# Kernel tuning notes

Measured on AMD Instinct MI355X. Metric: run time of the kernel, lower is better.

Reference implementation:

```python
import jax, jax.numpy as jnp
import numpy as np

# ---- config (matches init_kwargs) ----
L_LEVELS = 10          # int(log(8192/16)/log(2)) + 1
LEVEL_DIM = 4
BASE_RES = 16
LOG2_T = 21
BOUND = 2.0            # contract() output bound
DENSITY_BIAS = -1.0
RGB_PADDING = 0.001
DEG_VIEW = 4
PRIME1 = np.uint32(2654435761)
PRIME2 = np.uint32(805459861)


def _grid_meta():
    # torch-ngp GridEncoder layout: per-level scale = base*2^l - 1 (per_level_scale=2),
    # resolution = base*2^l, params = min(2^21, (res+1)^3) rounded up to multiple of 8.
    offsets, scales, res_list, sizes = [0], [], [], []
    for l in range(L_LEVELS):
        res = BASE_RES * (2 ** l)
        scales.append(float(res - 1))
        n = min(2 ** LOG2_T, (res + 1) ** 3)
        n = int(np.ceil(n / 8) * 8)
        res_list.append(res)
        sizes.append(n)
        offsets.append(offsets[-1] + n)
    return scales, res_list, sizes, offsets

GRID_SCALES, GRID_RES, GRID_SIZES, GRID_OFFSETS = _grid_meta()
TOTAL_PARAMS = GRID_OFFSETS[-1]  # 14995560
CORNERS = np.array([[(c >> d) & 1 for d in range(3)] for c in range(8)], dtype=np.int32)


def contract(x):
    # mipnerf360 contraction, output in [-2, 2]
    eps = jnp.finfo(x.dtype).eps
    x_mag_sq = jnp.maximum(eps, jnp.sum(x * x, axis=-1, keepdims=True))
    return jnp.where(x_mag_sq <= 1.0, x, ((2.0 * jnp.sqrt(x_mag_sq) - 1.0) / x_mag_sq) * x)


def pos_enc(x):
    # coord.pos_enc with identity, min_deg=0, max_deg=DEG_VIEW -> dim 3 + 3*2*4 = 27
    scales = 2.0 ** jnp.arange(DEG_VIEW, dtype=x.dtype)
    xb = (x[..., None, :] * scales[:, None]).reshape(x.shape[:-1] + (3 * DEG_VIEW,))
    four = jnp.sin(jnp.concatenate([xb, xb + 0.5 * jnp.pi], axis=-1))
    return jnp.concatenate([x, four], axis=-1)


def grid_encode(x01, embeddings):
    # x01: [N,3] in [0,1]; embeddings: [TOTAL_PARAMS, LEVEL_DIM]
    feats = []
    for l in range(L_LEVELS):
        pos = x01 * GRID_SCALES[l] + 0.5  # align_corners=False
        pos_floor = jnp.floor(pos)
        frac = pos - pos_floor            # trilinear weights, differentiable in x01
        pg = pos_floor.astype(jnp.int32)  # [N,3]
        res1 = GRID_RES[l] + 1
        size = GRID_SIZES[l]
        use_hash = (res1 ** 3) > size
        lvl_emb = embeddings[GRID_OFFSETS[l]:GRID_OFFSETS[l] + size]
        acc = jnp.zeros(x01.shape[:-1] + (LEVEL_DIM,), x01.dtype)
        for c in range(8):
            off = CORNERS[c]
            corner = pg + off[None, :]
            if use_hash:
                cu = corner.astype(jnp.uint32)
                idx = (cu[:, 0] ^ (cu[:, 1] * PRIME1) ^ (cu[:, 2] * PRIME2)) % jnp.uint32(size)
                idx = idx.astype(jnp.int32)
            else:
                idx = corner[:, 0] + corner[:, 1] * res1 + corner[:, 2] * (res1 * res1)
            w = jnp.prod(jnp.where(off[None, :] == 1, frac, 1.0 - frac), axis=-1)  # [N]
            acc = acc + w[:, None] * lvl_emb[idx]
        feats.append(acc)
    return jnp.concatenate(feats, axis=-1)  # [N, 40]


def setup_inputs() -> dict:
    key = jax.random.key(0)
    ks = jax.random.split(key, 10)
    R, S = 2048, 32
    coords = jax.random.normal(ks[0], (R, S, 3), jnp.float32) * 1.5
    viewdirs = jax.random.normal(ks[1], (R, 3), jnp.float32)
    viewdirs = viewdirs / jnp.linalg.norm(viewdirs, axis=-1, keepdims=True)
    embeddings = (jax.random.uniform(ks[2], (TOTAL_PARAMS, LEVEL_DIM), jnp.float32) * 2.0 - 1.0) * 1e-4

    def lin(k, fan_in, fan_out):
        k1, k2 = jax.random.split(k)
        lim = 1.0 / np.sqrt(fan_in)
        w = jax.random.uniform(k1, (fan_in, fan_out), jnp.float32, -lim, lim)
        b = jax.random.uniform(k2, (fan_out,), jnp.float32, -lim, lim)
        return w, b

    w_d1, b_d1 = lin(ks[3], L_LEVELS * LEVEL_DIM, 64)
    w_d2, b_d2 = lin(ks[4], 64, 256)
    DIR_DIM = 3 + 3 * 2 * DEG_VIEW  # 27
    w_r0, b_r0 = lin(ks[5], 256 + DIR_DIM, 256)          # 283 -> 256
    w_r1, b_r1 = lin(ks[6], 256 + 256 + DIR_DIM, 256)    # skip concat: 539 -> 256
    w_rgb, b_rgb = lin(ks[7], 256, 3)
    return dict(coords=coords, viewdirs=viewdirs, embeddings=embeddings,
                w_d1=w_d1, b_d1=b_d1, w_d2=w_d2, b_d2=b_d2,
                w_r0=w_r0, b_r0=b_r0, w_r1=w_r1, b_r1=b_r1,
                w_rgb=w_rgb, b_rgb=b_rgb)


def reference(coords, viewdirs, embeddings, w_d1, b_d1, w_d2, b_d2,
              w_r0, b_r0, w_r1, b_r1, w_rgb, b_rgb):
    shape = coords.shape[:-1]  # (rays, samples)
    cw = contract(coords) / BOUND          # coords_warped, in [-1, 1]
    x01 = (cw.reshape(-1, 3) + BOUND) / (2.0 * BOUND)  # encoder normalization with bound=2
    feats = grid_encode(x01, embeddings)               # [N, 40]
    h = jax.nn.relu(feats @ w_d1 + b_d1)
    x = h @ w_d2 + b_d2                                # [N, 256]
    raw_density = x[:, 0].reshape(shape)
    density = jax.nn.softplus(raw_density + DENSITY_BIAS)
    bottleneck = x.reshape(shape + (256,))
    dir_enc = pos_enc(viewdirs)                        # [rays, 27]
    dir_enc = jnp.broadcast_to(dir_enc[..., None, :], shape + (dir_enc.shape[-1],))
    inp = jnp.concatenate([bottleneck, dir_enc], axis=-1)  # [rays, S, 283]
    y = jax.nn.relu(inp @ w_r0 + b_r0)
    y = jnp.concatenate([y, inp], axis=-1)             # skip at layer i == skip_layer_dir == 0
    y = jax.nn.relu(y @ w_r1 + b_r1)
    rgb = jax.nn.sigmoid(y @ w_rgb + b_rgb)            # rgb_premultiplier=1, rgb_bias=0
    rgb = rgb * (1.0 + 2.0 * RGB_PADDING) - RGB_PADDING
    return cw, density, rgb
```

## Files before the change

kernel.cpp:

```cpp
#include <hip/hip_runtime.h>
#include <math.h>

#define NS 65536
#define NRAYS 2048

typedef __attribute__((ext_vector_type(8))) short short8;
typedef __attribute__((ext_vector_type(4))) float f32x4;
typedef unsigned short u16;

#define OFF_FEATS 0ull
#define OFF_HBF   10485760ull
#define OFF_XBF   18874368ull
#define OFF_YBF   52428800ull
#define OFF_DW0   85983232ull
#define OFF_DW1   88080384ull
#define OFF_WD2T  90177536ull
#define OFF_WR0T  90210304ull
#define OFF_WR1T  90341376ull

#define OUT_DENS 196608
#define OUT_RGB  262144

__device__ __forceinline__ u16 f2b(float f) {
    unsigned u = __builtin_bit_cast(unsigned, f);
    return (u16)((u + 0x7FFFu + ((u >> 16) & 1u)) >> 16);
}

__global__ __launch_bounds__(256) void cvt_weights(
    const float* __restrict__ w_d2, const float* __restrict__ w_r0,
    const float* __restrict__ w_r1, u16* __restrict__ wd2t,
    u16* __restrict__ wr0t, u16* __restrict__ wr1t)
{
    int idx = blockIdx.x * 256 + threadIdx.x;
    if (idx < 16384)  wd2t[idx] = f2b(w_d2[(idx & 63)  * 256 + (idx >> 6)]);
    if (idx < 65536)  wr0t[idx] = f2b(w_r0[(idx & 255) * 256 + (idx >> 8)]);
    if (idx < 131072) wr1t[idx] = f2b(w_r1[(idx & 511) * 256 + (idx >> 9)]);
}

__global__ __launch_bounds__(256) void dir_kernel(
    const float* __restrict__ viewdirs,
    const float* __restrict__ w_r0, const float* __restrict__ b_r0,
    const float* __restrict__ w_r1, const float* __restrict__ b_r1,
    float* __restrict__ dirW0, float* __restrict__ dirW1)
{
    __shared__ float de[27];
    int ray = blockIdx.x, t = threadIdx.x;
    if (t < 27) {
        float v;
        if (t < 3) v = viewdirs[3*ray + t];
        else {
            int k = (t - 3) % 12;
            float b = viewdirs[3*ray + (k % 3)] * (float)(1 << (k / 3));
            v = (t < 15) ? sinf(b) : sinf(b + 1.5707964f);
        }
        de[t] = v;
    }
    __syncthreads();
    float a0 = b_r0[t], a1 = b_r1[t];
#pragma unroll
    for (int d = 0; d < 27; ++d) {
        a0 = fmaf(de[d], w_r0[(256+d)*256 + t], a0);
        a1 = fmaf(de[d], w_r1[(512+d)*256 + t], a1);
    }
    dirW0[ray*256 + t] = a0;
    dirW1[ray*256 + t] = a1;
}

__global__ __launch_bounds__(256) void encode_kernel(
    const float* __restrict__ coords, const float* __restrict__ emb,
    float* __restrict__ cw_out, float* __restrict__ featsT)
{
    int t = threadIdx.x;
    int l = blockIdx.x >> 8;
    int i = ((blockIdx.x & 255) << 8) + t;
    float x = coords[3*i], y = coords[3*i+1], z = coords[3*i+2];
    float m2 = fmaxf(x*x + y*y + z*z, 1.1920928955078125e-07f);
    float cx = x, cy = y, cz = z;
    if (m2 > 1.0f) { float s = (2.0f*sqrtf(m2) - 1.0f)/m2; cx*=s; cy*=s; cz*=s; }
    cx *= 0.5f; cy *= 0.5f; cz *= 0.5f;
    if (l == 0) { cw_out[3*i]=cx; cw_out[3*i+1]=cy; cw_out[3*i+2]=cz; }
    float u0 = (cx + 2.0f)*0.25f, u1 = (cy + 2.0f)*0.25f, u2 = (cz + 2.0f)*0.25f;

    int res = 16 << l;
    int res1 = res + 1;
    float scale = (float)(res - 1);
    unsigned off = (l >= 3) ? 315496u + (unsigned)(l-3)*2097152u
                            : (l == 0 ? 0u : (l == 1 ? 4920u : 40864u));
    float p0 = u0*scale + 0.5f, p1 = u1*scale + 0.5f, p2 = u2*scale + 0.5f;
    float f0 = floorf(p0), f1 = floorf(p1), f2 = floorf(p2);
    float fr0 = p0-f0, fr1 = p1-f1, fr2 = p2-f2;
    unsigned g0 = (unsigned)(int)f0, g1 = (unsigned)(int)f1, g2 = (unsigned)(int)f2;
    float a0=0.f, a1=0.f, a2=0.f, a3=0.f;
    bool use_hash = (l >= 3);
#pragma unroll
    for (int c = 0; c < 8; ++c) {
        unsigned ox = c & 1u, oy = (c >> 1) & 1u, oz = (c >> 2) & 1u;
        unsigned qx = g0 + ox, qy = g1 + oy, qz = g2 + oz;
        unsigned idx;
        if (use_hash) idx = (qx ^ (qy*2654435761u) ^ (qz*805459861u)) & 2097151u;
        else          idx = qx + qy*(unsigned)res1 + qz*(unsigned)(res1*res1);
        const float4 e = *(const float4*)(emb + 4u*(off + idx));
        float w = (ox ? fr0 : 1.0f-fr0) * (oy ? fr1 : 1.0f-fr1) * (oz ? fr2 : 1.0f-fr2);
        a0 = fmaf(w, e.x, a0); a1 = fmaf(w, e.y, a1);
        a2 = fmaf(w, e.z, a2); a3 = fmaf(w, e.w, a3);
    }
    featsT[(4*l+0)*NS + i] = a0;
    featsT[(4*l+1)*NS + i] = a1;
    featsT[(4*l+2)*NS + i] = a2;
    featsT[(4*l+3)*NS + i] = a3;
}

__global__ __launch_bounds__(256) void gemm_d1_kernel(
    const float* __restrict__ featsT, const float* __restrict__ w_d1,
    const float* __restrict__ b_d1, const float* __restrict__ w_d2,
    const float* __restrict__ b_d2, u16* __restrict__ h_bf,
    float* __restrict__ dens)
{
    __shared__ float As[40][256];
    __shared__ float Ws[40*64];
    __shared__ float wc0[64];
    int t = threadIdx.x;
    int m0 = blockIdx.x * 256;
#pragma unroll
    for (int k = 0; k < 40; ++k) As[k][t] = featsT[k*NS + m0 + t];
#pragma unroll
    for (int i = 0; i < 10; ++i) Ws[i*256 + t] = w_d1[i*256 + t];
    if (t < 64) wc0[t] = w_d2[t*256];
    __syncthreads();
    int tn = t & 3, tm = t >> 2;
    float acc[4][16] = {};
#pragma unroll
    for (int k = 0; k < 40; ++k) {
        float4 a = *(const float4*)&As[k][tm*4];
        float av[4] = {a.x, a.y, a.z, a.w};
        const float4* wp = (const float4*)&Ws[k*64 + tn*16];
#pragma unroll
        for (int r = 0; r < 4; ++r) {
            float4 w = wp[r];
            float wv[4] = {w.x, w.y, w.z, w.w};
#pragma unroll
            for (int ii = 0; ii < 4; ++ii)
#pragma unroll
                for (int cc = 0; cc < 4; ++cc)
                    acc[ii][r*4+cc] = fmaf(av[ii], wv[cc], acc[ii][r*4+cc]);
        }
    }
    float p[4] = {0.f, 0.f, 0.f, 0.f};
#pragma unroll
    for (int jj = 0; jj < 16; ++jj) {
        int j = tn*16 + jj;
        float bj = b_d1[j], w0 = wc0[j];
#pragma unroll
        for (int ii = 0; ii < 4; ++ii) {
            float h = fmaxf(acc[ii][jj] + bj, 0.f);
            acc[ii][jj] = h;
            p[ii] = fmaf(h, w0, p[ii]);
        }
    }
#pragma unroll
    for (int ii = 0; ii < 4; ++ii) {
        int s = m0 + tm*4 + ii;
        unsigned u[8];
#pragma unroll
        for (int q = 0; q < 8; ++q)
            u[q] = (unsigned)f2b(acc[ii][2*q]) | ((unsigned)f2b(acc[ii][2*q+1]) << 16);
        uint4 v0 = {u[0], u[1], u[2], u[3]};
        uint4 v1 = {u[4], u[5], u[6], u[7]};
        *(uint4*)(h_bf + (size_t)s*64 + tn*16)     = v0;
        *(uint4*)(h_bf + (size_t)s*64 + tn*16 + 8) = v1;
    }
#pragma unroll
    for (int ii = 0; ii < 4; ++ii) {
        p[ii] += __shfl_xor(p[ii], 1, 64);
        p[ii] += __shfl_xor(p[ii], 2, 64);
    }
    if (tn == 0) {
        float b0 = b_d2[0];
#pragma unroll
        for (int ii = 0; ii < 4; ++ii) {
            float z = p[ii] + b0 - 1.0f;
            dens[m0 + tm*4 + ii] = fmaxf(z, 0.f) + log1pf(expf(-fabsf(z)));
        }
    }
}

#define MFMA __builtin_amdgcn_mfma_f32_16x16x32_bf16

__global__ __launch_bounds__(256) void mfma_d2(
    const u16* __restrict__ h_bf, const u16* __restrict__ wt,
    const float* __restrict__ b_d2, u16* __restrict__ xbf)
{
    int t = threadIdx.x, lane = t & 63, w = t >> 6;
    int m0 = blockIdx.x*128 + w*32;
    int rl = lane & 15, kg = (lane >> 4) * 8;
    f32x4 zero = {0.f,0.f,0.f,0.f};
    f32x4 acc[2][16];
#pragma unroll
    for (int a = 0; a < 2; ++a)
#pragma unroll
        for (int b = 0; b < 16; ++b) acc[a][b] = zero;
    const u16* pA0 = h_bf + (size_t)(m0 + rl)*64 + kg;
    const u16* pA1 = h_bf + (size_t)(m0 + 16 + rl)*64 + kg;
    const u16* pB  = wt + rl*64 + kg;
#pragma unroll
    for (int ks = 0; ks < 2; ++ks) {
        int kb = ks*32;
        short8 a0 = *(const short8*)(pA0 + kb);
        short8 a1 = *(const short8*)(pA1 + kb);
#pragma unroll
        for (int nt = 0; nt < 16; ++nt) {
            short8 b = *(const short8*)(pB + nt*1024 + kb);
            acc[0][nt] = MFMA(a0, b, acc[0][nt], 0, 0, 0);
            acc[1][nt] = MFMA(a1, b, acc[1][nt], 0, 0, 0);
        }
    }
    int ro = (lane >> 4) * 4;
#pragma unroll
    for (int nt = 0; nt < 16; ++nt) {
        int col = nt*16 + rl;
        float bias = b_d2[col];
#pragma unroll
        for (int mt = 0; mt < 2; ++mt)
#pragma unroll
            for (int r = 0; r < 4; ++r)
                xbf[(size_t)(m0 + mt*16 + ro + r)*256 + col] = f2b(acc[mt][nt][r] + bias);
    }
}

__global__ __launch_bounds__(256) void mfma_r0(
    const u16* __restrict__ xbf, const u16* __restrict__ wt,
    const float* __restrict__ dirW0, u16* __restrict__ ybf)
{
    int t = threadIdx.x, lane = t & 63, w = t >> 6;
    int m0 = blockIdx.x*128 + w*32;
    int rl = lane & 15, kg = (lane >> 4) * 8;
    f32x4 zero = {0.f,0.f,0.f,0.f};
    f32x4 acc[2][16];
#pragma unroll
    for (int a = 0; a < 2; ++a)
#pragma unroll
        for (int b = 0; b < 16; ++b) acc[a][b] = zero;
    const u16* pA0 = xbf + (size_t)(m0 + rl)*256 + kg;
    const u16* pA1 = xbf + (size_t)(m0 + 16 + rl)*256 + kg;
    const u16* pB  = wt + rl*256 + kg;
#pragma unroll
    for (int ks = 0; ks < 8; ++ks) {
        int kb = ks*32;
        short8 a0 = *(const short8*)(pA0 + kb);
        short8 a1 = *(const short8*)(pA1 + kb);
#pragma unroll
        for (int nt = 0; nt < 16; ++nt) {
            short8 b = *(const short8*)(pB + nt*4096 + kb);
            acc[0][nt] = MFMA(a0, b, acc[0][nt], 0, 0, 0);
            acc[1][nt] = MFMA(a1, b, acc[1][nt], 0, 0, 0);
        }
    }
    const float* dir = dirW0 + (m0 >> 5)*256;
    int ro = (lane >> 4) * 4;
#pragma unroll
    for (int nt = 0; nt < 16; ++nt) {
        int col = nt*16 + rl;
        float bias = dir[col];
#pragma unroll
        for (int mt = 0; mt < 2; ++mt)
#pragma unroll
            for (int r = 0; r < 4; ++r)
                ybf[(size_t)(m0 + mt*16 + ro + r)*256 + col] =
                    f2b(fmaxf(acc[mt][nt][r] + bias, 0.f));
    }
}

__global__ __launch_bounds__(256) void mfma_r1(
    const u16* __restrict__ ybf, const u16* __restrict__ xbf,
    const u16* __restrict__ wt, const float* __restrict__ dirW1,
    const float* __restrict__ w_rgb, const float* __restrict__ b_rgb,
    float* __restrict__ rgb)
{
    int t = threadIdx.x, lane = t & 63, w = t >> 6;
    int m0 = blockIdx.x*128 + w*32;
    int rl = lane & 15, kg = (lane >> 4) * 8;
    f32x4 zero = {0.f,0.f,0.f,0.f};
    f32x4 acc[2][16];
#pragma unroll
    for (int a = 0; a < 2; ++a)
#pragma unroll
        for (int b = 0; b < 16; ++b) acc[a][b] = zero;
    const u16* pAy0 = ybf + (size_t)(m0 + rl)*256 + kg;
    const u16* pAy1 = ybf + (size_t)(m0 + 16 + rl)*256 + kg;
    const u16* pAx0 = xbf + (size_t)(m0 + rl)*256 + kg;
    const u16* pAx1 = xbf + (size_t)(m0 + 16 + rl)*256 + kg;
    const u16* pB   = wt + rl*512 + kg;
#pragma unroll
    for (int ks = 0; ks < 16; ++ks) {
        int kb = ks*32;
        int kl = (ks & 7)*32;
        short8 a0 = (ks < 8) ? *(const short8*)(pAy0 + kl) : *(const short8*)(pAx0 + kl);
        short8 a1 = (ks < 8) ? *(const short8*)(pAy1 + kl) : *(const short8*)(pAx1 + kl);
#pragma unroll
        for (int nt = 0; nt < 16; ++nt) {
            short8 b = *(const short8*)(pB + nt*8192 + kb);
            acc[0][nt] = MFMA(a0, b, acc[0][nt], 0, 0, 0);
            acc[1][nt] = MFMA(a1, b, acc[1][nt], 0, 0, 0);
        }
    }
    const float* dir = dirW1 + (m0 >> 5)*256;
    float p[2][4][3];
#pragma unroll
    for (int mt = 0; mt < 2; ++mt)
#pragma unroll
        for (int r = 0; r < 4; ++r)
            p[mt][r][0] = p[mt][r][1] = p[mt][r][2] = 0.f;
#pragma unroll
    for (int nt = 0; nt < 16; ++nt) {
        int col = nt*16 + rl;
        float dv = dir[col];
        float w0 = w_rgb[col*3], w1 = w_rgb[col*3+1], w2 = w_rgb[col*3+2];
#pragma unroll
        for (int mt = 0; mt < 2; ++mt)
#pragma unroll
            for (int r = 0; r < 4; ++r) {
                float y1 = fmaxf(acc[mt][nt][r] + dv, 0.f);
                p[mt][r][0] = fmaf(y1, w0, p[mt][r][0]);
                p[mt][r][1] = fmaf(y1, w1, p[mt][r][1]);
                p[mt][r][2] = fmaf(y1, w2, p[mt][r][2]);
            }
    }
#pragma unroll
    for (int mask = 1; mask < 16; mask <<= 1)
#pragma unroll
        for (int mt = 0; mt < 2; ++mt)
#pragma unroll
            for (int r = 0; r < 4; ++r)
#pragma unroll
                for (int c = 0; c < 3; ++c)
                    p[mt][r][c] += __shfl_xor(p[mt][r][c], mask, 64);
    if (rl == 0) {
        int ro = (lane >> 4) * 4;
#pragma unroll
        for (int mt = 0; mt < 2; ++mt)
#pragma unroll
            for (int r = 0; r < 4; ++r) {
                int row = m0 + mt*16 + ro + r;
#pragma unroll
                for (int c = 0; c < 3; ++c) {
                    float v = p[mt][r][c] + b_rgb[c];
                    float sg = 1.0f / (1.0f + expf(-v));
                    rgb[row*3 + c] = sg * 1.002f - 0.001f;
                }
            }
    }
}

extern "C" void kernel_launch(void* const* d_in, const int* in_sizes, int n_in,
                              void* d_out, int out_size, void* d_ws, size_t ws_size,
                              hipStream_t stream)
{
    const float* coords   = (const float*)d_in[0];
    const float* viewdirs = (const float*)d_in[1];
    const float* emb      = (const float*)d_in[2];
    const float* w_d1     = (const float*)d_in[3];
    const float* b_d1     = (const float*)d_in[4];
    const float* w_d2     = (const float*)d_in[5];
    const float* b_d2     = (const float*)d_in[6];
    const float* w_r0     = (const float*)d_in[7];
    const float* b_r0     = (const float*)d_in[8];
    const float* w_r1     = (const float*)d_in[9];
    const float* b_r1     = (const float*)d_in[10];
    const float* w_rgb    = (const float*)d_in[11];
    const float* b_rgb    = (const float*)d_in[12];

    float* out  = (float*)d_out;
    float* cw   = out;
    float* dens = out + OUT_DENS;
    float* rgb  = out + OUT_RGB;

    char* wsB = (char*)d_ws;
    float* featsT = (float*)(wsB + OFF_FEATS);
    u16*   h_bf   = (u16*)(wsB + OFF_HBF);
    u16*   xbf    = (u16*)(wsB + OFF_XBF);
    u16*   ybf    = (u16*)(wsB + OFF_YBF);
    float* dirW0  = (float*)(wsB + OFF_DW0);
    float* dirW1  = (float*)(wsB + OFF_DW1);
    u16*   wd2t   = (u16*)(wsB + OFF_WD2T);
    u16*   wr0t   = (u16*)(wsB + OFF_WR0T);
    u16*   wr1t   = (u16*)(wsB + OFF_WR1T);

    cvt_weights<<<512, 256, 0, stream>>>(w_d2, w_r0, w_r1, wd2t, wr0t, wr1t);
    dir_kernel<<<NRAYS, 256, 0, stream>>>(viewdirs, w_r0, b_r0, w_r1, b_r1, dirW0, dirW1);
    encode_kernel<<<2560, 256, 0, stream>>>(coords, emb, cw, featsT);
    gemm_d1_kernel<<<NS/256, 256, 0, stream>>>(featsT, w_d1, b_d1, w_d2, b_d2, h_bf, dens);
    mfma_d2<<<NS/128, 256, 0, stream>>>(h_bf, wd2t, b_d2, xbf);
    mfma_r0<<<NS/128, 256, 0, stream>>>(xbf, wr0t, dirW0, ybf);
    mfma_r1<<<NS/128, 256, 0, stream>>>(ybf, xbf, wr1t, dirW1, w_rgb, b_rgb, rgb);
}
```

Baseline: 508.9 us.

## Fuse r0 and r1 MLP layers via LDS-staged activations; coalesce d2 stores

```diff
diff --git a/kernel.cpp b/kernel.cpp
--- a/kernel.cpp
+++ b/kernel.cpp
@@ -11,7 +11,6 @@
 #define OFF_FEATS 0ull
 #define OFF_HBF   10485760ull
 #define OFF_XBF   18874368ull
-#define OFF_YBF   52428800ull
 #define OFF_DW0   85983232ull
 #define OFF_DW1   88080384ull
 #define OFF_WD2T  90177536ull
@@ -190,6 +189,7 @@
     const u16* __restrict__ h_bf, const u16* __restrict__ wt,
     const float* __restrict__ b_d2, u16* __restrict__ xbf)
 {
+    __shared__ u16 xt[4][8192];
     int t = threadIdx.x, lane = t & 63, w = t >> 6;
     int m0 = blockIdx.x*128 + w*32;
     int rl = lane & 15, kg = (lane >> 4) * 8;
@@ -215,6 +215,7 @@
         }
     }
     int ro = (lane >> 4) * 4;
+    u16* xw = xt[w];
 #pragma unroll
     for (int nt = 0; nt < 16; ++nt) {
         int col = nt*16 + rl;
@@ -222,104 +223,127 @@
 #pragma unroll
         for (int mt = 0; mt < 2; ++mt)
 #pragma unroll
-            for (int r = 0; r < 4; ++r)
-                xbf[(size_t)(m0 + mt*16 + ro + r)*256 + col] = f2b(acc[mt][nt][r] + bias);
-    }
-}
-
-__global__ __launch_bounds__(256) void mfma_r0(
-    const u16* __restrict__ xbf, const u16* __restrict__ wt,
-    const float* __restrict__ dirW0, u16* __restrict__ ybf)
-{
+            for (int r = 0; r < 4; ++r) {
+                int row = mt*16 + ro + r;
+                unsigned byte = (unsigned)(row*512 + col*2) ^ ((unsigned)(row & 7) << 4);
+                xw[byte >> 1] = f2b(acc[mt][nt][r] + bias);
+            }
+    }
+#pragma unroll
+    for (int it = 0; it < 16; ++it) {
+        unsigned flat = it*1024u + (unsigned)lane*16u;
+        unsigned row = flat >> 9, off = flat & 511u;
+        unsigned lb = flat ^ ((row & 7u) << 4);
+        short8 v = *(const short8*)((const char*)xw + lb);
+        *(short8*)(xbf + (size_t)(m0 + row)*256 + (off >> 1)) = v;
+    }
+}
+
+__global__ __launch_bounds__(256) void mfma_tail(
+    const u16* __restrict__ xbf, const u16* __restrict__ w0t,
+    const u16* __restrict__ w1t, const float* __restrict__ dirW0,
+    const float* __restrict__ dirW1, const float* __restrict__ w_rgb,
+    const float* __restrict__ b_rgb, float* __restrict__ rgb)
+{
+    __shared__ u16 yt[4][8192];
     int t = threadIdx.x, lane = t & 63, w = t >> 6;
     int m0 = blockIdx.x*128 + w*32;
     int rl = lane & 15, kg = (lane >> 4) * 8;
+    int ro = (lane >> 4) * 4;
     f32x4 zero = {0.f,0.f,0.f,0.f};
-    f32x4 acc[2][16];
-#pragma unroll
-    for (int a = 0; a < 2; ++a)
-#pragma unroll
-        for (int b = 0; b < 16; ++b) acc[a][b] = zero;
     const u16* pA0 = xbf + (size_t)(m0 + rl)*256 + kg;
     const u16* pA1 = xbf + (size_t)(m0 + 16 + rl)*256 + kg;
-    const u16* pB  = wt + rl*256 + kg;
-#pragma unroll
-    for (int ks = 0; ks < 8; ++ks) {
-        int kb = ks*32;
-        short8 a0 = *(const short8*)(pA0 + kb);
-        short8 a1 = *(const short8*)(pA1 + kb);
+
+    f32x4 acc0[2][16];
+#pragma unroll
+    for (int a = 0; a < 2; ++a)
+#pragma unroll
+        for (int b = 0; b < 16; ++b) acc0[a][b] = zero;
+    {
+        const u16* pB = w0t + rl*256 + kg;
+#pragma unroll
+        for (int ks = 0; ks < 8; ++ks) {
+            int kb = ks*32;
+            short8 a0 = *(const short8*)(pA0 + kb);
+            short8 a1 = *(const short8*)(pA1 + kb);
+#pragma unroll
+            for (int nt = 0; nt < 16; ++nt) {
+                short8 b = *(const short8*)(pB + nt*4096 + kb);
+                acc0[0][nt] = MFMA(a0, b, acc0[0][nt], 0, 0, 0);
+                acc0[1][nt] = MFMA(a1, b, acc0[1][nt], 0, 0, 0);
+            }
+        }
+    }
+    {
+        const float* dir0 = dirW0 + (m0 >> 5)*256;
+        u16* yw = yt[w];
 #pragma unroll
         for (int nt = 0; nt < 16; ++nt) {
-            short8 b = *(const short8*)(pB + nt*4096 + kb);
-            acc[0][nt] = MFMA(a0, b, acc[0][nt], 0, 0, 0);
-            acc[1][nt] = MFMA(a1, b, acc[1][nt], 0, 0, 0);
-        }
-    }
-    const float* dir = dirW0 + (m0 >> 5)*256;
-    int ro = (lane >> 4) * 4;
+            int col = nt*16 + rl;
+            float bias = dir0[col];
+#pragma unroll
+            for (int mt = 0; mt < 2; ++mt)
+#pragma unroll
+                for (int r = 0; r < 4; ++r) {
+                    int row = mt*16 + ro + r;
+                    unsigned byte = (unsigned)(row*512 + col*2) ^ ((unsigned)(row & 7) << 4);
+                    yw[byte >> 1] = f2b(fmaxf(acc0[mt][nt][r] + bias, 0.f));
+                }
+        }
+    }
+    f32x4 acc1[2][16];
+#pragma unroll
+    for (int a = 0; a < 2; ++a)
+#pragma unroll
+        for (int b = 0; b < 16; ++b) acc1[a][b] = zero;
+    {
+        const u16* pB = w1t + rl*512;
+        const char* ywc = (const char*)yt[w];
+        unsigned sw = ((unsigned)(rl & 7)) << 4;
+#pragma unroll
+        for (int ks = 0; ks < 8; ++ks) {
+            int kb = ks*32;
+            unsigned base = (unsigned)((kb + kg)*2);
+            short8 a0 = *(const short8*)(ywc + (((unsigned)(rl*512)       + base) ^ sw));
+            short8 a1 = *(const short8*)(ywc + (((unsigned)((16+rl)*512)  + base) ^ sw));
+#pragma unroll
+            for (int nt = 0; nt < 16; ++nt) {
+                short8 b = *(const short8*)(pB + nt*8192 + kg + kb);
+                acc1[0][nt] = MFMA(a0, b, acc1[0][nt], 0, 0, 0);
+                acc1[1][nt] = MFMA(a1, b, acc1[1][nt], 0, 0, 0);
+            }
+        }
+#pragma unroll
+        for (int ks = 8; ks < 16; ++ks) {
+            int kb = ks*32;
+            int kl = kb - 256;
+            short8 a0 = *(const short8*)(pA0 + kl);
+            short8 a1 = *(const short8*)(pA1 + kl);
+#pragma unroll
+            for (int nt = 0; nt < 16; ++nt) {
+                short8 b = *(const short8*)(pB + nt*8192 + kg + kb);
+                acc1[0][nt] = MFMA(a0, b, acc1[0][nt], 0, 0, 0);
+                acc1[1][nt] = MFMA(a1, b, acc1[1][nt], 0, 0, 0);
+            }
+        }
+    }
+    const float* dir1 = dirW1 + (m0 >> 5)*256;
+    float p[2][4][3];
+#pragma unroll
+    for (int mt = 0; mt < 2; ++mt)
+#pragma unroll
+        for (int r = 0; r < 4; ++r)
+            p[mt][r][0] = p[mt][r][1] = p[mt][r][2] = 0.f;
 #pragma unroll
     for (int nt = 0; nt < 16; ++nt) {
         int col = nt*16 + rl;
-        float bias = dir[col];
+        float dv = dir1[col];
+        float w0 = w_rgb[col*3], w1 = w_rgb[col*3+1], w2 = w_rgb[col*3+2];
 #pragma unroll
         for (int mt = 0; mt < 2; ++mt)
 #pragma unroll
-            for (int r = 0; r < 4; ++r)
-                ybf[(size_t)(m0 + mt*16 + ro + r)*256 + col] =
-                    f2b(fmaxf(acc[mt][nt][r] + bias, 0.f));
-    }
-}
-
-__global__ __launch_bounds__(256) void mfma_r1(
-    const u16* __restrict__ ybf, const u16* __restrict__ xbf,
-    const u16* __restrict__ wt, const float* __restrict__ dirW1,
-    const float* __restrict__ w_rgb, const float* __restrict__ b_rgb,
-    float* __restrict__ rgb)
-{
-    int t = threadIdx.x, lane = t & 63, w = t >> 6;
-    int m0 = blockIdx.x*128 + w*32;
-    int rl = lane & 15, kg = (lane >> 4) * 8;
-    f32x4 zero = {0.f,0.f,0.f,0.f};
-    f32x4 acc[2][16];
-#pragma unroll
-    for (int a = 0; a < 2; ++a)
-#pragma unroll
-        for (int b = 0; b < 16; ++b) acc[a][b] = zero;
-    const u16* pAy0 = ybf + (size_t)(m0 + rl)*256 + kg;
-    const u16* pAy1 = ybf + (size_t)(m0 + 16 + rl)*256 + kg;
-    const u16* pAx0 = xbf + (size_t)(m0 + rl)*256 + kg;
-    const u16* pAx1 = xbf + (size_t)(m0 + 16 + rl)*256 + kg;
-    const u16* pB   = wt + rl*512 + kg;
-#pragma unroll
-    for (int ks = 0; ks < 16; ++ks) {
-        int kb = ks*32;
-        int kl = (ks & 7)*32;
-        short8 a0 = (ks < 8) ? *(const short8*)(pAy0 + kl) : *(const short8*)(pAx0 + kl);
-        short8 a1 = (ks < 8) ? *(const short8*)(pAy1 + kl) : *(const short8*)(pAx1 + kl);
-#pragma unroll
-        for (int nt = 0; nt < 16; ++nt) {
-            short8 b = *(const short8*)(pB + nt*8192 + kb);
-            acc[0][nt] = MFMA(a0, b, acc[0][nt], 0, 0, 0);
-            acc[1][nt] = MFMA(a1, b, acc[1][nt], 0, 0, 0);
-        }
-    }
-    const float* dir = dirW1 + (m0 >> 5)*256;
-    float p[2][4][3];
-#pragma unroll
-    for (int mt = 0; mt < 2; ++mt)
-#pragma unroll
-        for (int r = 0; r < 4; ++r)
-            p[mt][r][0] = p[mt][r][1] = p[mt][r][2] = 0.f;
-#pragma unroll
-    for (int nt = 0; nt < 16; ++nt) {
-        int col = nt*16 + rl;
-        float dv = dir[col];
-        float w0 = w_rgb[col*3], w1 = w_rgb[col*3+1], w2 = w_rgb[col*3+2];
-#pragma unroll
-        for (int mt = 0; mt < 2; ++mt)
-#pragma unroll
             for (int r = 0; r < 4; ++r) {
-                float y1 = fmaxf(acc[mt][nt][r] + dv, 0.f);
+                float y1 = fmaxf(acc1[mt][nt][r] + dv, 0.f);
                 p[mt][r][0] = fmaf(y1, w0, p[mt][r][0]);
                 p[mt][r][1] = fmaf(y1, w1, p[mt][r][1]);
                 p[mt][r][2] = fmaf(y1, w2, p[mt][r][2]);
@@ -335,7 +359,6 @@
                 for (int c = 0; c < 3; ++c)
                     p[mt][r][c] += __shfl_xor(p[mt][r][c], mask, 64);
     if (rl == 0) {
-        int ro = (lane >> 4) * 4;
 #pragma unroll
         for (int mt = 0; mt < 2; ++mt)
 #pragma unroll
@@ -378,7 +401,6 @@
     float* featsT = (float*)(wsB + OFF_FEATS);
     u16*   h_bf   = (u16*)(wsB + OFF_HBF);
     u16*   xbf    = (u16*)(wsB + OFF_XBF);
-    u16*   ybf    = (u16*)(wsB + OFF_YBF);
     float* dirW0  = (float*)(wsB + OFF_DW0);
     float* dirW1  = (float*)(wsB + OFF_DW1);
     u16*   wd2t   = (u16*)(wsB + OFF_WD2T);
@@ -390,6 +412,5 @@
     encode_kernel<<<2560, 256, 0, stream>>>(coords, emb, cw, featsT);
     gemm_d1_kernel<<<NS/256, 256, 0, stream>>>(featsT, w_d1, b_d1, w_d2, b_d2, h_bf, dens);
     mfma_d2<<<NS/128, 256, 0, stream>>>(h_bf, wd2t, b_d2, xbf);
-    mfma_r0<<<NS/128, 256, 0, stream>>>(xbf, wr0t, dirW0, ybf);
-    mfma_r1<<<NS/128, 256, 0, stream>>>(ybf, xbf, wr1t, dirW1, w_rgb, b_rgb, rgb);
-}
+    mfma_tail<<<NS/128, 256, 0, stream>>>(xbf, wr0t, wr1t, dirW0, dirW1, w_rgb, b_rgb, rgb);
+}
```

New measurement: 495.5 us. 1.03x faster.
